# Kernel optimization log

Hardware: AMD Instinct MI355X
Metric: run time of the kernel (lower is better)

Reference implementation:

```python
import jax, jax.numpy as jnp
import numpy as np

B, N, C_IN, C_OUT = 8, 4096, 64, 64
NEG_INF = -9e15
LEAKY_SLOPE = 0.01  # torch F.leaky_relu default


def setup_inputs() -> dict:
    key = jax.random.key(0)
    kx, ka, kw, kq, kk = jax.random.split(key, 5)
    X = jax.random.normal(kx, (B, N, C_IN), dtype=jnp.float32)
    A = jax.random.randint(ka, (N, N), 0, 2, dtype=jnp.int32)
    # xavier_uniform with gain=1.414 ~ scaled uniform; plain scaled normal is fine for a numeric reference
    def xavier(k, shape):
        fan_in, fan_out = shape
        bound = 1.414 * np.sqrt(6.0 / (fan_in + fan_out))
        return jax.random.uniform(k, shape, jnp.float32, -bound, bound)
    weight = xavier(kw, (C_IN, C_OUT))
    query = xavier(kq, (C_IN, C_OUT))
    key_p = xavier(kk, (C_IN, C_OUT))
    return {"X": X, "A": A, "weight": weight, "query": query, "key_p": key_p}


def reference(X, A, weight, query, key_p):
    n = X.shape[1]
    idx = jnp.arange(n)
    adj = A.at[idx, idx].set(1)  # add self-loops
    out = jnp.einsum('bni,io->bno', X, weight)
    q = jnp.einsum('bni,io->bno', X, query)
    k = jnp.einsum('bni,io->bno', X, key_p)
    att = jnp.einsum('bnd,bmd->bnm', q, k)          # QK^T, (B,N,N)
    att = jax.nn.leaky_relu(att, LEAKY_SLOPE)
    att = jnp.where(adj[None, :, :] > 0, att, NEG_INF)
    att = jax.nn.softmax(att, axis=-1)
    # dropout p=0 and/or eval mode -> identity
    return jnp.einsum('bnm,bmo->bno', att, out)
```

## Files before the change

### kernel.cpp

```cpp
#include <hip/hip_runtime.h>
#include <stdint.h>

#define BATCH 8
#define NN 4096
#define CC 64
#define MASKV -1.0e30f
#define LOG2E 1.4426950408889634f

typedef _Float16 half8 __attribute__((ext_vector_type(8)));
typedef _Float16 half4 __attribute__((ext_vector_type(4)));
typedef __fp16 fp16x2 __attribute__((ext_vector_type(2)));
typedef float f32x4 __attribute__((ext_vector_type(4)));
typedef float f32x16 __attribute__((ext_vector_type(16)));

typedef __attribute__((address_space(1))) const unsigned int gu32;
typedef __attribute__((address_space(3))) unsigned int lu32;
#define GLL16(gp, lp) __builtin_amdgcn_global_load_lds( \
    (gu32*)(uintptr_t)(gp), (lu32*)(unsigned)(uintptr_t)(lp), 16, 0, 0)

__device__ __forceinline__ unsigned pk_rtz(float a, float b) {
    union { fp16x2 h; unsigned u; } r;
    r.h = __builtin_amdgcn_cvt_pkrtz(a, b);
    return r.u;
}

__global__ __launch_bounds__(256) void gat_prep(
    const float* __restrict__ X, const float* __restrict__ W0,
    const float* __restrict__ Wq, const float* __restrict__ Wk,
    const int* __restrict__ A,
    _Float16* __restrict__ qh, _Float16* __restrict__ kb,
    _Float16* __restrict__ vt, unsigned short* __restrict__ M16)
{
    __shared__ alignas(16) _Float16 WTh[3][64][72];
    __shared__ alignas(16) _Float16 WTl[3][64][72];
    const int t = threadIdx.x;
    if (blockIdx.x >= 512) {
        const int row = blockIdx.x - 512;
        const int4* ap = (const int4*)(A + (size_t)row * NN + t * 16);
        unsigned m = 0;
        #pragma unroll
        for (int j = 0; j < 4; ++j) {
            int4 a = ap[j];
            m |= (a.x != 0 ? 1u : 0u) << (4*j);
            m |= (a.y != 0 ? 1u : 0u) << (4*j + 1);
            m |= (a.z != 0 ? 1u : 0u) << (4*j + 2);
            m |= (a.w != 0 ? 1u : 0u) << (4*j + 3);
        }
        if (t == (row >> 4)) m |= 1u << (row & 15);
        M16[(size_t)row * 256 + t] = (unsigned short)m;
        return;
    }
    const float* Ws[3] = {W0, Wq, Wk};
    for (int e = t; e < 4096; e += 256) {
        int k = e >> 6, c = e & 63;
        #pragma unroll
        for (int m = 0; m < 3; ++m) {
            float w = Ws[m][e];
            _Float16 hi = (_Float16)w;
            WTh[m][c][k] = hi;
            WTl[m][c][k] = (_Float16)(w - (float)hi);
        }
    }
    __syncthreads();
    const int lane = t & 63, wv = t >> 6;
    const int cl = lane & 15, g = lane >> 4;
    int tile = blockIdx.x * 4 + wv;
    int gr = tile * 16;
    const float* xr = X + (size_t)(gr + cl) * CC;
    half8 xh[2], xl[2];
    #pragma unroll
    for (int kf = 0; kf < 2; ++kf) {
        f32x4 a0 = *(const f32x4*)(xr + g*8 + kf*32);
        f32x4 a1 = *(const f32x4*)(xr + g*8 + kf*32 + 4);
        half8 h, l;
        #pragma unroll
        for (int j = 0; j < 4; ++j) {
            _Float16 h0 = (_Float16)a0[j], h1 = (_Float16)a1[j];
            h[j]   = h0; l[j]   = (_Float16)(a0[j] - (float)h0);
            h[j+4] = h1; l[j+4] = (_Float16)(a1[j] - (float)h1);
        }
        xh[kf] = h; xl[kf] = l;
    }
    #pragma unroll
    for (int mat = 1; mat <= 2; ++mat) {
        #pragma unroll
        for (int nt = 0; nt < 4; ++nt) {
            f32x4 acc = {0.f, 0.f, 0.f, 0.f};
            #pragma unroll
            for (int kf = 0; kf < 2; ++kf) {
                half8 bh = *(const half8*)&WTh[mat][nt*16 + cl][g*8 + kf*32];
                half8 bl = *(const half8*)&WTl[mat][nt*16 + cl][g*8 + kf*32];
                acc = __builtin_amdgcn_mfma_f32_16x16x32_f16(xh[kf], bh, acc, 0, 0, 0);
                acc = __builtin_amdgcn_mfma_f32_16x16x32_f16(xl[kf], bh, acc, 0, 0, 0);
                acc = __builtin_amdgcn_mfma_f32_16x16x32_f16(xh[kf], bl, acc, 0, 0, 0);
            }
            #pragma unroll
            for (int i = 0; i < 4; ++i) {
                size_t off = (size_t)(gr + 4*g + i) * CC + nt*16 + cl;
                if (mat == 1) qh[off] = (_Float16)(acc[i] * LOG2E);
                else          kb[off] = (_Float16)acc[i];
            }
        }
    }
    {
        int b = gr >> 12, n0 = gr & (NN - 1);
        #pragma unroll
        for (int mt = 0; mt < 4; ++mt) {
            f32x4 acc = {0.f, 0.f, 0.f, 0.f};
            #pragma unroll
            for (int kf = 0; kf < 2; ++kf) {
                half8 ah = *(const half8*)&WTh[0][mt*16 + cl][g*8 + kf*32];
                half8 al = *(const half8*)&WTl[0][mt*16 + cl][g*8 + kf*32];
                acc = __builtin_amdgcn_mfma_f32_16x16x32_f16(ah, xh[kf], acc, 0, 0, 0);
                acc = __builtin_amdgcn_mfma_f32_16x16x32_f16(al, xh[kf], acc, 0, 0, 0);
                acc = __builtin_amdgcn_mfma_f32_16x16x32_f16(ah, xl[kf], acc, 0, 0, 0);
            }
            #pragma unroll
            for (int i = 0; i < 4; ++i) {
                int co = mt*16 + 4*g + i;
                vt[((size_t)b * CC + co) * NN + n0 + cl] = (_Float16)acc[i];
            }
        }
    }
}

__global__ __launch_bounds__(256, 3) void gat_attn(
    const _Float16* __restrict__ qg,
    const _Float16* __restrict__ kf16, const _Float16* __restrict__ vtb,
    const unsigned long long* __restrict__ M,
    _Float16* __restrict__ po, float2* __restrict__ pml)
{
    __shared__ alignas(16) _Float16 Kt[2][64][64];
    __shared__ alignas(16) _Float16 Vt[2][64][64];
    __shared__ alignas(8) uint2 LUT[16];
    const int t = threadIdx.x;
    const int lane = t & 63, wv = t >> 6;
    const int q32 = lane & 31, hi = lane >> 5;
    const int blk = blockIdx.x;
    const int b  = blk & 7;
    const int sp = (blk >> 3) & 3;
    const int qb = blk >> 5;
    const int Q0 = qb * 128 + wv * 32;
    const int c0 = sp * 16;
    const int swz = (q32 & 7) << 4;

    if (t < 16) {
        unsigned n = t;
        LUT[n] = make_uint2(((n & 1u) ? 0x0000FFFFu : 0u) | ((n & 2u) ? 0xFFFF0000u : 0u),
                            ((n & 4u) ? 0x0000FFFFu : 0u) | ((n & 8u) ? 0xFFFF0000u : 0u));
    }

    const int lrow = lane >> 3;
    const int lcol = ((lane & 7) * 16) ^ (lrow << 4);
    const bool isK = (wv < 2);
    const int seg = isK ? wv : (wv - 2);
    const char* gsrc0 = isK
        ? (const char*)(kf16 + (size_t)b * NN * CC)
            + (size_t)c0 * 8192 + (size_t)seg * 4096 + lrow * 128 + lcol
        : (const char*)(vtb + (size_t)b * CC * NN)
            + (size_t)c0 * 128 + ((size_t)(seg * 32 + lrow)) * 8192 + lcol;
    const int istride = isK ? 1024 : 65536;
    const int cstride = isK ? 8192 : 128;

    auto stage = [&](int rel, int bufi) {
        const char* s = gsrc0 + (size_t)rel * cstride;
        char* d = isK ? ((char*)&Kt[bufi][0][0] + seg * 4096)
                      : ((char*)&Vt[bufi][0][0] + seg * 4096);
        #pragma unroll
        for (int i = 0; i < 4; ++i)
            GLL16(s + i * istride, d + i * 1024);
    };
    auto pkmax = [](unsigned a, unsigned b) {
        unsigned d;
        asm("v_pk_max_f16 %0, %1, %2" : "=v"(d) : "v"(a), "v"(b));
        return d;
    };

    half8 qf[4];
    {
        const _Float16* qr = qg + ((size_t)b * NN + Q0 + q32) * CC + hi * 8;
        #pragma unroll
        for (int kf = 0; kf < 4; ++kf) qf[kf] = *(const half8*)(qr + kf * 16);
    }
    const unsigned long long* Mrow = M + (size_t)(Q0 + q32) * 64 + c0;

    f32x16 o0 = {}, o1 = {};
    float m_run = 0.f, l_run = 0.f;

    stage(0, 0);
    unsigned long long cm = Mrow[0];
    __syncthreads();

    for (int kc = 0; kc < 16; ++kc) {
        const int cur = kc & 1;
        unsigned long long pmn = 0;
        if (kc < 15) {
            stage(kc + 1, cur ^ 1);
            pmn = Mrow[kc + 1];
        }

        const char* kbase = (const char*)&Kt[cur][0][0] + q32 * 128;
        __builtin_amdgcn_s_setprio(1);
        f32x16 s0 = {}, s1 = {};
        #pragma unroll
        for (int kf = 0; kf < 4; ++kf) {
            const int col = (kf * 32 + hi * 16) ^ swz;
            half8 ka0 = *(const half8*)(kbase + col);
            half8 ka1 = *(const half8*)(kbase + 4096 + col);
            s0 = __builtin_amdgcn_mfma_f32_32x32x16_f16(ka0, qf[kf], s0, 0, 0, 0);
            s1 = __builtin_amdgcn_mfma_f32_32x32x16_f16(ka1, qf[kf], s1, 0, 0, 0);
        }
        __builtin_amdgcn_s_setprio(0);

        const unsigned wlo = (unsigned)cm, whi = (unsigned)(cm >> 32);

        {
            unsigned run0 = 0u, run1 = 0u;
            #pragma unroll
            for (int a = 0; a < 4; ++a) {
                uint2 e0 = LUT[(wlo >> (8*a + 4*hi)) & 15u];
                uint2 e1 = LUT[(whi >> (8*a + 4*hi)) & 15u];
                run0 = pkmax(run0, pk_rtz(s0[4*a],   s0[4*a+1]) & e0.x);
                run0 = pkmax(run0, pk_rtz(s0[4*a+2], s0[4*a+3]) & e0.y);
                run1 = pkmax(run1, pk_rtz(s1[4*a],   s1[4*a+1]) & e1.x);
                run1 = pkmax(run1, pk_rtz(s1[4*a+2], s1[4*a+3]) & e1.y);
            }
            union { unsigned u; fp16x2 h; } tu; tu.u = pkmax(run0, run1);
            float mx = fmaxf((float)tu.h[0], (float)tu.h[1]);
            mx = fmaxf(mx, __shfl_xor(mx, 32));
            if (__any(mx > m_run + 8.0f)) {
                float nm = fmaxf(m_run, mx);
                float alpha = __builtin_amdgcn_exp2f(m_run - nm);
                m_run = nm;
                l_run *= alpha;
                #pragma unroll
                for (int i = 0; i < 16; ++i) { o0[i] *= alpha; o1[i] *= alpha; }
            }
        }
        unsigned wp[16];
        #pragma unroll
        for (int a = 0; a < 4; ++a) {
            uint2 e0 = LUT[(wlo >> (8*a + 4*hi)) & 15u];
            uint2 e1 = LUT[(whi >> (8*a + 4*hi)) & 15u];
            float p0 = __builtin_amdgcn_exp2f(fmaxf(s0[4*a]   - m_run, fmaf(0.01f, s0[4*a],   -m_run)));
            float p1 = __builtin_amdgcn_exp2f(fmaxf(s0[4*a+1] - m_run, fmaf(0.01f, s0[4*a+1], -m_run)));
            float p2 = __builtin_amdgcn_exp2f(fmaxf(s0[4*a+2] - m_run, fmaf(0.01f, s0[4*a+2], -m_run)));
            float p3 = __builtin_amdgcn_exp2f(fmaxf(s0[4*a+3] - m_run, fmaf(0.01f, s0[4*a+3], -m_run)));
            wp[2*a]   = pk_rtz(p0, p1) & e0.x;
            wp[2*a+1] = pk_rtz(p2, p3) & e0.y;
            float p4 = __builtin_amdgcn_exp2f(fmaxf(s1[4*a]   - m_run, fmaf(0.01f, s1[4*a],   -m_run)));
            float p5 = __builtin_amdgcn_exp2f(fmaxf(s1[4*a+1] - m_run, fmaf(0.01f, s1[4*a+1], -m_run)));
            float p6 = __builtin_amdgcn_exp2f(fmaxf(s1[4*a+2] - m_run, fmaf(0.01f, s1[4*a+2], -m_run)));
            float p7 = __builtin_amdgcn_exp2f(fmaxf(s1[4*a+3] - m_run, fmaf(0.01f, s1[4*a+3], -m_run)));
            wp[8+2*a]   = pk_rtz(p4, p5) & e1.x;
            wp[8+2*a+1] = pk_rtz(p6, p7) & e1.y;
        }
        {
            union { unsigned u; fp16x2 h; } z; z.u = 0u;
            fp16x2 acc = z.h;
            #pragma unroll
            for (int j4 = 0; j4 < 4; ++j4) {
                union { unsigned u; fp16x2 h; } x0, x1, x2, x3;
                x0.u = wp[4*j4]; x1.u = wp[4*j4+1]; x2.u = wp[4*j4+2]; x3.u = wp[4*j4+3];
                acc += (x0.h + x1.h) + (x2.h + x3.h);
            }
            l_run += (float)acc[0] + (float)acc[1];
        }
        #pragma unroll
        for (int g4 = 0; g4 < 4; ++g4) {
            unsigned w0 = wp[4*g4+0], w1 = wp[4*g4+1];
            unsigned w2 = wp[4*g4+2], w3 = wp[4*g4+3];
            unsigned u = hi ? w0 : w2;
            unsigned v = hi ? w1 : w3;
            unsigned su = (unsigned)__shfl_xor((int)u, 32);
            unsigned sv = (unsigned)__shfl_xor((int)v, 32);
            wp[4*g4+0] = hi ? su : w0;
            wp[4*g4+1] = hi ? sv : w1;
            wp[4*g4+2] = hi ? w2 : su;
            wp[4*g4+3] = hi ? w3 : sv;
        }
        const char* vb = (const char*)&Vt[cur][0][0] + q32 * 128;
        __builtin_amdgcn_s_setprio(1);
        #pragma unroll
        for (int kc4 = 0; kc4 < 4; ++kc4) {
            union { unsigned u[4]; half8 h; } pb;
            pb.u[0] = wp[4*kc4+0]; pb.u[1] = wp[4*kc4+1];
            pb.u[2] = wp[4*kc4+2]; pb.u[3] = wp[4*kc4+3];
            const int col = (kc4 * 32 + hi * 16) ^ swz;
            half8 vf0 = *(const half8*)(vb + col);
            half8 vf1 = *(const half8*)(vb + 4096 + col);
            o0 = __builtin_amdgcn_mfma_f32_32x32x16_f16(vf0, pb.h, o0, 0, 0, 0);
            o1 = __builtin_amdgcn_mfma_f32_32x32x16_f16(vf1, pb.h, o1, 0, 0, 0);
        }
        __builtin_amdgcn_s_setprio(0);
        cm = pmn;
        if (kc < 15) __syncthreads();
    }

    float lt = l_run + __shfl_xor(l_run, 32);
    float invl = (lt > 0.f) ? 1.0f / lt : 0.f;
    size_t base = (size_t)sp * (BATCH * NN) + (size_t)b * NN + Q0 + q32;
    _Float16* orow = po + base * 64;
    #pragma unroll
    for (int a = 0; a < 4; ++a) {
        {
            uint2 ow = { pk_rtz(o0[4*a] * invl, o0[4*a+1] * invl),
                         pk_rtz(o0[4*a+2] * invl, o0[4*a+3] * invl) };
            *(uint2*)(orow + 8*a + 4*hi) = ow;
        }
        {
            uint2 ow = { pk_rtz(o1[4*a] * invl, o1[4*a+1] * invl),
                         pk_rtz(o1[4*a+2] * invl, o1[4*a+3] * invl) };
            *(uint2*)(orow + 32 + 8*a + 4*hi) = ow;
        }
    }
    if (hi == 0) pml[base] = make_float2(m_run, lt);
}

__global__ __launch_bounds__(256) void gat_comb(
    const _Float16* __restrict__ po, const float2* __restrict__ pml,
    float* __restrict__ out)
{
    int gid = blockIdx.x * 256 + threadIdx.x;
    int row = gid >> 4;
    int col = (gid & 15) * 4;
    float2 ml[4];
    float Mx = MASKV;
    #pragma unroll
    for (int s = 0; s < 4; ++s) {
        ml[s] = pml[s * (BATCH * NN) + row];
        Mx = fmaxf(Mx, ml[s].x);
    }
    float w[4], den = 0.f;
    #pragma unroll
    for (int s = 0; s < 4; ++s) {
        w[s] = __builtin_amdgcn_exp2f(ml[s].x - Mx) * ml[s].y;
        den += w[s];
    }
    float inv = 1.0f / den;
    float acc[4] = {};
    #pragma unroll
    for (int s = 0; s < 4; ++s) {
        const _Float16* p = po + ((size_t)s * (BATCH * NN) + row) * 64 + col;
        float a = w[s] * inv;
        half4 v = *(const half4*)(p);
        #pragma unroll
        for (int j = 0; j < 4; ++j) acc[j] += a * (float)v[j];
    }
    f32x4 r = {acc[0], acc[1], acc[2], acc[3]};
    *(f32x4*)(out + (size_t)row * 64 + col) = r;
}

extern "C" void kernel_launch(void* const* d_in, const int* in_sizes, int n_in,
                              void* d_out, int out_size, void* d_ws, size_t ws_size,
                              hipStream_t stream) {
    const float* X  = (const float*)d_in[0];
    const int*   A  = (const int*)d_in[1];
    const float* W0 = (const float*)d_in[2];
    const float* Wq = (const float*)d_in[3];
    const float* Wk = (const float*)d_in[4];
    float* out = (float*)d_out;
    char* ws = (char*)d_ws;
    const size_t SZ = (size_t)BATCH * NN * CC * 2;
    _Float16* qh  = (_Float16*)(ws);
    _Float16* kbf = (_Float16*)(ws + SZ);
    _Float16* vtb = (_Float16*)(ws + 2*SZ);
    char* Mbase = ws + 3*SZ;
    _Float16* po = (_Float16*)(Mbase + 2*1024*1024);
    float2* pml  = (float2*)(Mbase + 2*1024*1024 + 4*SZ);

    hipLaunchKernelGGL(gat_prep, dim3(4608), dim3(256), 0, stream,
                       X, W0, Wq, Wk, A, qh, kbf, vtb, (unsigned short*)Mbase);
    hipLaunchKernelGGL(gat_attn, dim3(1024), dim3(256), 0, stream, qh, kbf, vtb,
                       (const unsigned long long*)Mbase, po, pml);
    hipLaunchKernelGGL(gat_comb, dim3(2048), dim3(256), 0, stream, po, pml, out);
}
```

Baseline: 187.9 us.

## Interleave softmax exp with PV MFMAs per chunk and raise occupancy to 4

```diff
diff --git a/kernel.cpp b/kernel.cpp
--- a/kernel.cpp
+++ b/kernel.cpp
@@ -124,7 +124,7 @@
     }
 }
 
-__global__ __launch_bounds__(256, 3) void gat_attn(
+__global__ __launch_bounds__(256, 4) void gat_attn(
     const _Float16* __restrict__ qg,
     const _Float16* __restrict__ kf16, const _Float16* __restrict__ vtb,
     const unsigned long long* __restrict__ M,
@@ -237,62 +237,54 @@
                 for (int i = 0; i < 16; ++i) { o0[i] *= alpha; o1[i] *= alpha; }
             }
         }
-        unsigned wp[16];
-        #pragma unroll
-        for (int a = 0; a < 4; ++a) {
-            uint2 e0 = LUT[(wlo >> (8*a + 4*hi)) & 15u];
-            uint2 e1 = LUT[(whi >> (8*a + 4*hi)) & 15u];
-            float p0 = __builtin_amdgcn_exp2f(fmaxf(s0[4*a]   - m_run, fmaf(0.01f, s0[4*a],   -m_run)));
-            float p1 = __builtin_amdgcn_exp2f(fmaxf(s0[4*a+1] - m_run, fmaf(0.01f, s0[4*a+1], -m_run)));
-            float p2 = __builtin_amdgcn_exp2f(fmaxf(s0[4*a+2] - m_run, fmaf(0.01f, s0[4*a+2], -m_run)));
-            float p3 = __builtin_amdgcn_exp2f(fmaxf(s0[4*a+3] - m_run, fmaf(0.01f, s0[4*a+3], -m_run)));
-            wp[2*a]   = pk_rtz(p0, p1) & e0.x;
-            wp[2*a+1] = pk_rtz(p2, p3) & e0.y;
-            float p4 = __builtin_amdgcn_exp2f(fmaxf(s1[4*a]   - m_run, fmaf(0.01f, s1[4*a],   -m_run)));
-            float p5 = __builtin_amdgcn_exp2f(fmaxf(s1[4*a+1] - m_run, fmaf(0.01f, s1[4*a+1], -m_run)));
-            float p6 = __builtin_amdgcn_exp2f(fmaxf(s1[4*a+2] - m_run, fmaf(0.01f, s1[4*a+2], -m_run)));
-            float p7 = __builtin_amdgcn_exp2f(fmaxf(s1[4*a+3] - m_run, fmaf(0.01f, s1[4*a+3], -m_run)));
-            wp[8+2*a]   = pk_rtz(p4, p5) & e1.x;
-            wp[8+2*a+1] = pk_rtz(p6, p7) & e1.y;
-        }
-        {
-            union { unsigned u; fp16x2 h; } z; z.u = 0u;
-            fp16x2 acc = z.h;
-            #pragma unroll
-            for (int j4 = 0; j4 < 4; ++j4) {
-                union { unsigned u; fp16x2 h; } x0, x1, x2, x3;
-                x0.u = wp[4*j4]; x1.u = wp[4*j4+1]; x2.u = wp[4*j4+2]; x3.u = wp[4*j4+3];
-                acc += (x0.h + x1.h) + (x2.h + x3.h);
-            }
-            l_run += (float)acc[0] + (float)acc[1];
-        }
+
+        const char* vb = (const char*)&Vt[cur][0][0] + q32 * 128;
+        union UHH { unsigned u; fp16x2 h; };
+        UHH zz; zz.u = 0u;
+        fp16x2 lacc = zz.h;
         #pragma unroll
         for (int g4 = 0; g4 < 4; ++g4) {
-            unsigned w0 = wp[4*g4+0], w1 = wp[4*g4+1];
-            unsigned w2 = wp[4*g4+2], w3 = wp[4*g4+3];
-            unsigned u = hi ? w0 : w2;
-            unsigned v = hi ? w1 : w3;
+            const unsigned wm = (g4 < 2) ? wlo : whi;
+            const int a0 = (g4 & 1) * 2;
+            unsigned w[4];
+            #pragma unroll
+            for (int aa = 0; aa < 2; ++aa) {
+                const int a = a0 + aa;
+                uint2 e = LUT[(wm >> (8*a + 4*hi)) & 15u];
+                float x0, x1, x2, x3;
+                if (g4 < 2) { x0 = s0[4*a]; x1 = s0[4*a+1]; x2 = s0[4*a+2]; x3 = s0[4*a+3]; }
+                else        { x0 = s1[4*a]; x1 = s1[4*a+1]; x2 = s1[4*a+2]; x3 = s1[4*a+3]; }
+                float p0 = __builtin_amdgcn_exp2f(fmaxf(x0 - m_run, fmaf(0.01f, x0, -m_run)));
+                float p1 = __builtin_amdgcn_exp2f(fmaxf(x1 - m_run, fmaf(0.01f, x1, -m_run)));
+                float p2 = __builtin_amdgcn_exp2f(fmaxf(x2 - m_run, fmaf(0.01f, x2, -m_run)));
+                float p3 = __builtin_amdgcn_exp2f(fmaxf(x3 - m_run, fmaf(0.01f, x3, -m_run)));
+                w[2*aa]   = pk_rtz(p0, p1) & e.x;
+                w[2*aa+1] = pk_rtz(p2, p3) & e.y;
+            }
+            {
+                UHH x0, x1, x2, x3;
+                x0.u = w[0]; x1.u = w[1]; x2.u = w[2]; x3.u = w[3];
+                lacc += (x0.h + x1.h) + (x2.h + x3.h);
+            }
+            unsigned u = hi ? w[0] : w[2];
+            unsigned v = hi ? w[1] : w[3];
             unsigned su = (unsigned)__shfl_xor((int)u, 32);
             unsigned sv = (unsigned)__shfl_xor((int)v, 32);
-            wp[4*g4+0] = hi ? su : w0;
-            wp[4*g4+1] = hi ? sv : w1;
-            wp[4*g4+2] = hi ? w2 : su;
-            wp[4*g4+3] = hi ? w3 : sv;
-        }
-        const char* vb = (const char*)&Vt[cur][0][0] + q32 * 128;
-        __builtin_amdgcn_s_setprio(1);
-        #pragma unroll
-        for (int kc4 = 0; kc4 < 4; ++kc4) {
             union { unsigned u[4]; half8 h; } pb;
-            pb.u[0] = wp[4*kc4+0]; pb.u[1] = wp[4*kc4+1];
-            pb.u[2] = wp[4*kc4+2]; pb.u[3] = wp[4*kc4+3];
-            const int col = (kc4 * 32 + hi * 16) ^ swz;
+            pb.u[0] = hi ? su : w[0];
+            pb.u[1] = hi ? sv : w[1];
+            pb.u[2] = hi ? w[2] : su;
+            pb.u[3] = hi ? w[3] : sv;
+            const int col = (g4 * 32 + hi * 16) ^ swz;
             half8 vf0 = *(const half8*)(vb + col);
             half8 vf1 = *(const half8*)(vb + 4096 + col);
+            __builtin_amdgcn_s_setprio(1);
             o0 = __builtin_amdgcn_mfma_f32_32x32x16_f16(vf0, pb.h, o0, 0, 0, 0);
             o1 = __builtin_amdgcn_mfma_f32_32x32x16_f16(vf1, pb.h, o1, 0, 0, 0);
-        }
-        __builtin_amdgcn_s_setprio(0);
+            __builtin_amdgcn_s_setprio(0);
+        }
+        l_run += (float)lacc[0] + (float)lacc[1];
+
         cm = pmn;
         if (kc < 15) __syncthreads();
     }
```

Measured after the change: 183.9 us. 1.02x faster.
